# Optimization experiments

Hardware: AMD Instinct MI355X
Metric: run time of the kernel (lower is better)

The kernel has to match this reference:

```python
import jax, jax.numpy as jnp
import numpy as np

B, T, D, M, N = 32, 24, 32, 32, 32
H = 32           # hidden_dim (must equal D due to .view in the torch code)
C = M * N        # number of independent per-cell LSTMs
K = 3            # conv kernel size, padding = K // 2


def setup_inputs() -> dict:
    key = jax.random.key(0)
    ks = jax.random.split(key, 7)
    s = 1.0 / np.sqrt(H)  # torch nn.LSTM default init scale
    return {
        "x": jax.random.normal(ks[0], (B, T, D, M, N), jnp.float32),
        "W_ih": jax.random.uniform(ks[1], (C, 4 * H, D), jnp.float32, -s, s),
        "W_hh": jax.random.uniform(ks[2], (C, 4 * H, H), jnp.float32, -s, s),
        "b_ih": jax.random.uniform(ks[3], (C, 4 * H), jnp.float32, -s, s),
        "b_hh": jax.random.uniform(ks[4], (C, 4 * H), jnp.float32, -s, s),
        "conv_w": jax.random.normal(ks[5], (1, H, K, K), jnp.float32) * 0.05,
        "conv_b": jax.random.normal(ks[6], (1,), jnp.float32) * 0.05,
    }


def _spatial_lstm(x, W_ih, W_hh, b_ih, b_hh):
    # x: (B,T,D,M,N) -> per-cell sequences (T,C,B,D)
    xf = x.reshape(B, T, D, C).transpose(1, 3, 0, 2)
    bias = (b_ih + b_hh)[:, None, :]  # (C,1,4H)

    def step(carry, xt):
        h, c = carry  # (C,B,H)
        g = (jnp.einsum('cbd,cgd->cbg', xt, W_ih)
             + jnp.einsum('cbh,cgh->cbg', h, W_hh) + bias)
        i, f, gg, o = jnp.split(g, 4, axis=-1)  # torch gate order i,f,g,o
        c = jax.nn.sigmoid(f) * c + jax.nn.sigmoid(i) * jnp.tanh(gg)
        h = jax.nn.sigmoid(o) * jnp.tanh(c)
        return (h, c), h

    h0 = jnp.zeros((C, B, H), x.dtype)
    _, hs = jax.lax.scan(step, (h0, h0), xf)  # hs: (T,C,B,H)
    # stack over cells, view back to grid: (B,T,H,M,N)
    return hs.transpose(2, 0, 3, 1).reshape(B, T, H, M, N)


def reference(x, W_ih, W_hh, b_ih, b_hh, conv_w, conv_b):
    spatial = _spatial_lstm(x, W_ih, W_hh, b_ih, b_hh)  # (B,T,H,M,N)
    y = jax.lax.conv_general_dilated(
        spatial.reshape(B * T, H, M, N), conv_w,
        window_strides=(1, 1), padding=[(K // 2, K // 2)] * 2,
        dimension_numbers=('NCHW', 'OIHW', 'NCHW'))
    y = y + conv_b[None, :, None, None]
    return jax.nn.sigmoid(y).reshape(B, T, -1, M, N)


if __name__ == "__main__":
    out = reference(**setup_inputs())
    print(out.shape)
```

## Files before the change

### kernel.cpp

```cpp
#include <hip/hip_runtime.h>

#define Bn 32
#define Tn 24
#define Dn 32
#define Hn 32
#define Cn 1024
#define DC (Dn*Cn)
#define TDC (Tn*Dn*Cn)
#define MP 34
#define PPXN (MP*MP)
#define IMGS (MP*MP*32)
#define SCALE 1.442695041f

typedef __attribute__((ext_vector_type(8))) short bf16x8;
typedef __attribute__((ext_vector_type(4))) float f32x4;

__device__ __forceinline__ unsigned cvt_pk(float lo, float hi) {
    unsigned r; asm("v_cvt_pk_bf16_f32 %0, %1, %2" : "=v"(r) : "v"(lo), "v"(hi)); return r;
}
__device__ __forceinline__ float lo16f(unsigned u) { return __builtin_bit_cast(float, u << 16); }
__device__ __forceinline__ float hi16f(unsigned u) { return __builtin_bit_cast(float, u & 0xffff0000u); }
__device__ __forceinline__ float rcp_(float x) { return __builtin_amdgcn_rcpf(x); }
__device__ __forceinline__ float exp2_(float x) { return __builtin_amdgcn_exp2f(x); }
__device__ __forceinline__ bf16x8 bc(int4 v) { return __builtin_bit_cast(bf16x8, v); }

struct __align__(16) LdsT {
    unsigned short Xh[2][2][32][48];
    unsigned short Xl[2][2][32][48];
    float Hf[2][2][32][36];
};

__global__ __launch_bounds__(512)
void zero_halo(unsigned short* __restrict__ sp) {
    int gid = blockIdx.x * 512 + threadIdx.x;
    if (gid >= 3072 * 132) return;
    int plane = gid / 132;
    int r = gid - plane * 132;
    int m, n;
    if (r < 34)       { m = 0;      n = r; }
    else if (r < 68)  { m = 33;     n = r - 34; }
    else if (r < 100) { m = r - 67; n = 0; }
    else              { m = r - 99; n = 33; }
    int4 z = {0, 0, 0, 0};
    *(int4*)(sp + ((size_t)plane * PPXN + m * MP + n) * 8) = z;
}

__global__ __launch_bounds__(256) __attribute__((amdgpu_waves_per_eu(3, 3)))
void lstm_k12(const float* __restrict__ x,
              const float* __restrict__ Wih,
              const float* __restrict__ Whh,
              const float* __restrict__ bih,
              const float* __restrict__ bhh,
              unsigned short* __restrict__ sp)
{
    __shared__ LdsT lds;
    const int tid  = threadIdx.x;
    const int lane = tid & 63;
    const int wave = tid >> 6;
    const int ci   = wave >> 1;
    const int half = wave & 1;
    const int l16  = lane & 15;
    const int kg   = lane >> 4;
    const int bid  = blockIdx.x;
    const int cellbase = (bid & 7) * 128 + (bid >> 3) * 2;
    const int cell = cellbase + ci;

    int4 wihh[4], wihl[4], whhh[4], whhl[4];
    float biasr[4];
#pragma unroll
    for (int q = 0; q < 4; ++q) {
        const int g = q * 32 + half * 16 + l16;
        const float* wp = Wih + (size_t)cell * 4096 + g * 32 + kg * 8;
        const float* hp = Whh + (size_t)cell * 4096 + g * 32 + kg * 8;
        float wv[8], hv[8];
#pragma unroll
        for (int j = 0; j < 8; ++j) { wv[j] = wp[j] * SCALE; hv[j] = hp[j] * SCALE; }
        unsigned a0 = cvt_pk(wv[0], wv[1]), a1 = cvt_pk(wv[2], wv[3]);
        unsigned a2 = cvt_pk(wv[4], wv[5]), a3 = cvt_pk(wv[6], wv[7]);
        wihh[q] = int4{(int)a0, (int)a1, (int)a2, (int)a3};
        wihl[q] = int4{(int)cvt_pk(wv[0] - lo16f(a0), wv[1] - hi16f(a0)),
                       (int)cvt_pk(wv[2] - lo16f(a1), wv[3] - hi16f(a1)),
                       (int)cvt_pk(wv[4] - lo16f(a2), wv[5] - hi16f(a2)),
                       (int)cvt_pk(wv[6] - lo16f(a3), wv[7] - hi16f(a3))};
        unsigned b0 = cvt_pk(hv[0], hv[1]), b1 = cvt_pk(hv[2], hv[3]);
        unsigned b2 = cvt_pk(hv[4], hv[5]), b3 = cvt_pk(hv[6], hv[7]);
        whhh[q] = int4{(int)b0, (int)b1, (int)b2, (int)b3};
        whhl[q] = int4{(int)cvt_pk(hv[0] - lo16f(b0), hv[1] - hi16f(b0)),
                       (int)cvt_pk(hv[2] - lo16f(b1), hv[3] - hi16f(b1)),
                       (int)cvt_pk(hv[4] - lo16f(b2), hv[5] - hi16f(b2)),
                       (int)cvt_pk(hv[6] - lo16f(b3), hv[7] - hi16f(b3))};
        biasr[q] = (bih[cell * 128 + g] + bhh[cell * 128 + g]) * SCALE;
    }

    const int sb = tid >> 3;
    const int d0 = (tid & 7) * 4;
    const float* xg0 = x + (size_t)sb * TDC + (size_t)d0 * Cn + cellbase;

    const int sm = cell >> 5, sn = cell & 31;
    const int ppx = (sm + 1) * MP + (sn + 1);
    unsigned short* spb = sp + ((size_t)(half * 16 + l16) * Tn * 4 + kg) * (PPXN * 8)
                             + (size_t)ppx * 8;

    float hD[8] = {};
    float cst[8] = {};
    float2 nx[4];
#pragma unroll
    for (int k = 0; k < 4; ++k) nx[k] = *(const float2*)(xg0 + k * Cn);

    for (int t = 0; t < Tn; ++t) {
        const int bufi = t & 1;
#pragma unroll
        for (int cc = 0; cc < 2; ++cc) {
            float f0 = cc ? nx[0].y : nx[0].x;
            float f1 = cc ? nx[1].y : nx[1].x;
            float f2 = cc ? nx[2].y : nx[2].x;
            float f3 = cc ? nx[3].y : nx[3].x;
            unsigned a0 = cvt_pk(f0, f1), a1 = cvt_pk(f2, f3);
            float r0 = f0 - lo16f(a0), r1 = f1 - hi16f(a0);
            float r2 = f2 - lo16f(a1), r3 = f3 - hi16f(a1);
            int2 hi2 = {(int)a0, (int)a1};
            int2 lo2 = {(int)cvt_pk(r0, r1), (int)cvt_pk(r2, r3)};
            *(int2*)&lds.Xh[bufi][cc][sb][d0] = hi2;
            *(int2*)&lds.Xl[bufi][cc][sb][d0] = lo2;
        }
#pragma unroll
        for (int i = 0; i < 8; ++i) {
            int mt = i >> 2, r = i & 3;
            lds.Hf[bufi][ci][mt * 16 + kg * 4 + r][half * 16 + l16] = hD[i];
        }
        __syncthreads();

        if (t < Tn - 1) {
#pragma unroll
            for (int k = 0; k < 4; ++k)
                nx[k] = *(const float2*)(xg0 + (size_t)(t + 1) * DC + k * Cn);
        }

        unsigned sphi0 = 0, sphi1 = 0, sphi2 = 0, sphi3 = 0;
#pragma unroll
        for (int mt = 0; mt < 2; ++mt) {
            int4 xfh = *(const int4*)&lds.Xh[bufi][ci][mt * 16 + l16][kg * 8];
            int4 xfl = *(const int4*)&lds.Xl[bufi][ci][mt * 16 + l16][kg * 8];
            const float* hp = &lds.Hf[bufi][ci][mt * 16 + l16][kg * 8];
            float4 ha = *(const float4*)hp;
            float4 hb = *(const float4*)(hp + 4);
            unsigned p0 = cvt_pk(ha.x, ha.y), p1 = cvt_pk(ha.z, ha.w);
            unsigned p2 = cvt_pk(hb.x, hb.y), p3 = cvt_pk(hb.z, hb.w);
            int4 hfh = int4{(int)p0, (int)p1, (int)p2, (int)p3};
            int4 hfl = int4{(int)cvt_pk(ha.x - lo16f(p0), ha.y - hi16f(p0)),
                            (int)cvt_pk(ha.z - lo16f(p1), ha.w - hi16f(p1)),
                            (int)cvt_pk(hb.x - lo16f(p2), hb.y - hi16f(p2)),
                            (int)cvt_pk(hb.z - lo16f(p3), hb.w - hi16f(p3))};
            if (mt == half) { sphi0 = p0; sphi1 = p1; sphi2 = p2; sphi3 = p3; }

            f32x4 acc[4];
#pragma unroll
            for (int q = 0; q < 4; ++q) {
                f32x4 a = {biasr[q], biasr[q], biasr[q], biasr[q]};
                a = __builtin_amdgcn_mfma_f32_16x16x32_bf16(bc(xfh), bc(wihh[q]), a, 0, 0, 0);
                a = __builtin_amdgcn_mfma_f32_16x16x32_bf16(bc(xfl), bc(wihh[q]), a, 0, 0, 0);
                a = __builtin_amdgcn_mfma_f32_16x16x32_bf16(bc(xfh), bc(wihl[q]), a, 0, 0, 0);
                a = __builtin_amdgcn_mfma_f32_16x16x32_bf16(bc(hfh), bc(whhh[q]), a, 0, 0, 0);
                a = __builtin_amdgcn_mfma_f32_16x16x32_bf16(bc(hfl), bc(whhh[q]), a, 0, 0, 0);
                a = __builtin_amdgcn_mfma_f32_16x16x32_bf16(bc(hfh), bc(whhl[q]), a, 0, 0, 0);
                acc[q] = a;
            }
#pragma unroll
            for (int r = 0; r < 4; ++r) {
                float gi = acc[0][r], gf = acc[1][r];
                float gg = acc[2][r], go = acc[3][r];
                float ig = rcp_(1.f + exp2_(-gi));
                float fg = rcp_(1.f + exp2_(-gf));
                float gt = 1.f - 2.f * rcp_(1.f + exp2_(gg + gg));
                float og = rcp_(1.f + exp2_(-go));
                float c  = fg * cst[mt * 4 + r] + ig * gt;
                cst[mt * 4 + r] = c;
                float tc = 1.f - 2.f * rcp_(1.f + exp2_((2.f * SCALE) * c));
                hD[mt * 4 + r] = og * tc;
            }
        }

        if (t > 0) {
            int4 sv = {(int)sphi0, (int)sphi1, (int)sphi2, (int)sphi3};
            *(int4*)(spb + (size_t)(t - 1) * IMGS) = sv;
        }
    }

#pragma unroll
    for (int i = 0; i < 8; ++i) {
        int mt = i >> 2, r = i & 3;
        lds.Hf[0][ci][mt * 16 + kg * 4 + r][half * 16 + l16] = hD[i];
    }
    __syncthreads();
    {
        const float* hp = &lds.Hf[0][ci][half * 16 + l16][kg * 8];
        float4 ha = *(const float4*)hp;
        float4 hb = *(const float4*)(hp + 4);
        int4 sv = {(int)cvt_pk(ha.x, ha.y), (int)cvt_pk(ha.z, ha.w),
                   (int)cvt_pk(hb.x, hb.y), (int)cvt_pk(hb.z, hb.w)};
        *(int4*)(spb + (size_t)(Tn - 1) * IMGS) = sv;
    }
}

__global__ __launch_bounds__(512, 4)
void conv_k4(const unsigned short* __restrict__ sp,
             const float* __restrict__ cw,
             const float* __restrict__ cb,
             float* __restrict__ out)
{
    __shared__ float wlds[9][32];
    const int tid = threadIdx.x;
    const int img = blockIdx.x;
    if (tid < 288) wlds[tid >> 5][tid & 31] = cw[(tid & 31) * 9 + (tid >> 5)];
    __syncthreads();
    const float bias = cb[0];
    float acc[2] = {bias, bias};
    int ppx[2];
#pragma unroll
    for (int pk = 0; pk < 2; ++pk) {
        int px = tid + pk * 512;
        ppx[pk] = ((px >> 5) + 1) * MP + (px & 31) + 1;
    }
#pragma unroll
    for (int hc = 0; hc < 4; ++hc) {
        float4 wa[9], wb[9];
#pragma unroll
        for (int tap = 0; tap < 9; ++tap) {
            wa[tap] = *(const float4*)&wlds[tap][hc * 8];
            wb[tap] = *(const float4*)&wlds[tap][hc * 8 + 4];
        }
        const unsigned short* plane = sp + (size_t)(img * 4 + hc) * (PPXN * 8);
#pragma unroll
        for (int pk = 0; pk < 2; ++pk) {
            const unsigned short* base = plane + (size_t)ppx[pk] * 8;
            float a = acc[pk];
#pragma unroll
            for (int dm = -1; dm <= 1; ++dm)
#pragma unroll
                for (int dn = -1; dn <= 1; ++dn) {
                    const int tap = (dm + 1) * 3 + (dn + 1);
                    int4 v = *(const int4*)(base + (dm * MP + dn) * 8);
                    float4 w0 = wa[tap], w1 = wb[tap];
                    a = fmaf(lo16f((unsigned)v.x), w0.x, a);
                    a = fmaf(hi16f((unsigned)v.x), w0.y, a);
                    a = fmaf(lo16f((unsigned)v.y), w0.z, a);
                    a = fmaf(hi16f((unsigned)v.y), w0.w, a);
                    a = fmaf(lo16f((unsigned)v.z), w1.x, a);
                    a = fmaf(hi16f((unsigned)v.z), w1.y, a);
                    a = fmaf(lo16f((unsigned)v.w), w1.z, a);
                    a = fmaf(hi16f((unsigned)v.w), w1.w, a);
                }
            acc[pk] = a;
        }
    }
#pragma unroll
    for (int pk = 0; pk < 2; ++pk)
        out[(size_t)img * 1024 + tid + pk * 512] = rcp_(1.f + exp2_(-SCALE * acc[pk]));
}

extern "C" void kernel_launch(void* const* d_in, const int* in_sizes, int n_in,
                              void* d_out, int out_size, void* d_ws, size_t ws_size,
                              hipStream_t stream) {
    const float* x   = (const float*)d_in[0];
    const float* Wih = (const float*)d_in[1];
    const float* Whh = (const float*)d_in[2];
    const float* bih = (const float*)d_in[3];
    const float* bhh = (const float*)d_in[4];
    const float* cw  = (const float*)d_in[5];
    const float* cb  = (const float*)d_in[6];
    float* out = (float*)d_out;
    unsigned short* sp = (unsigned short*)d_ws;

    zero_halo<<<792, 512, 0, stream>>>(sp);
    lstm_k12<<<512, 256, 0, stream>>>(x, Wih, Whh, bih, bhh, sp);
    conv_k4<<<Bn * Tn, 512, 0, stream>>>(sp, cw, cb, out);
}
```

Baseline: 103.9 us.

## Drop x low-part split, split MFMA chains, and use a lighter LDS barrier

Stops computing and storing the bf16 residual of x, which removes one MFMA per gate and the Xl LDS array. The input-projection and recurrent MFMA chains now go into separate accumulators that are added at the end, shortening the dependent chain. __syncthreads is replaced with a custom barrier that waits only on LDS counters, so the next-step global x prefetch is no longer waited on at the barrier. Pointer increments replace the per-step index math. The precision of x·W_ih drops to the bf16 hi part times the split weights.

```diff
diff --git a/kernel.cpp b/kernel.cpp
--- a/kernel.cpp
+++ b/kernel.cpp
@@ -24,9 +24,12 @@
 __device__ __forceinline__ float exp2_(float x) { return __builtin_amdgcn_exp2f(x); }
 __device__ __forceinline__ bf16x8 bc(int4 v) { return __builtin_bit_cast(bf16x8, v); }
 
+__device__ __forceinline__ void lds_barrier() {
+    asm volatile("s_waitcnt lgkmcnt(0)\n\ts_barrier" ::: "memory");
+}
+
 struct __align__(16) LdsT {
     unsigned short Xh[2][2][32][48];
-    unsigned short Xl[2][2][32][48];
     float Hf[2][2][32][36];
 };
 
@@ -46,7 +49,7 @@
 }
 
 __global__ __launch_bounds__(256) __attribute__((amdgpu_waves_per_eu(3, 3)))
-void lstm_k12(const float* __restrict__ x,
+void lstm_k15(const float* __restrict__ x,
               const float* __restrict__ Wih,
               const float* __restrict__ Whh,
               const float* __restrict__ bih,
@@ -95,11 +98,12 @@
     const int sb = tid >> 3;
     const int d0 = (tid & 7) * 4;
     const float* xg0 = x + (size_t)sb * TDC + (size_t)d0 * Cn + cellbase;
+    const float* xcur = xg0 + DC;
 
     const int sm = cell >> 5, sn = cell & 31;
     const int ppx = (sm + 1) * MP + (sn + 1);
-    unsigned short* spb = sp + ((size_t)(half * 16 + l16) * Tn * 4 + kg) * (PPXN * 8)
-                             + (size_t)ppx * 8;
+    unsigned short* spcur = sp + ((size_t)(half * 16 + l16) * Tn * 4 + kg) * (PPXN * 8)
+                               + (size_t)ppx * 8;
 
     float hD[8] = {};
     float cst[8] = {};
@@ -115,32 +119,26 @@
             float f1 = cc ? nx[1].y : nx[1].x;
             float f2 = cc ? nx[2].y : nx[2].x;
             float f3 = cc ? nx[3].y : nx[3].x;
-            unsigned a0 = cvt_pk(f0, f1), a1 = cvt_pk(f2, f3);
-            float r0 = f0 - lo16f(a0), r1 = f1 - hi16f(a0);
-            float r2 = f2 - lo16f(a1), r3 = f3 - hi16f(a1);
-            int2 hi2 = {(int)a0, (int)a1};
-            int2 lo2 = {(int)cvt_pk(r0, r1), (int)cvt_pk(r2, r3)};
+            int2 hi2 = {(int)cvt_pk(f0, f1), (int)cvt_pk(f2, f3)};
             *(int2*)&lds.Xh[bufi][cc][sb][d0] = hi2;
-            *(int2*)&lds.Xl[bufi][cc][sb][d0] = lo2;
         }
 #pragma unroll
         for (int i = 0; i < 8; ++i) {
             int mt = i >> 2, r = i & 3;
             lds.Hf[bufi][ci][mt * 16 + kg * 4 + r][half * 16 + l16] = hD[i];
         }
-        __syncthreads();
-
         if (t < Tn - 1) {
 #pragma unroll
             for (int k = 0; k < 4; ++k)
-                nx[k] = *(const float2*)(xg0 + (size_t)(t + 1) * DC + k * Cn);
-        }
+                nx[k] = *(const float2*)(xcur + k * Cn);
+            xcur += DC;
+        }
+        lds_barrier();
 
         unsigned sphi0 = 0, sphi1 = 0, sphi2 = 0, sphi3 = 0;
 #pragma unroll
         for (int mt = 0; mt < 2; ++mt) {
             int4 xfh = *(const int4*)&lds.Xh[bufi][ci][mt * 16 + l16][kg * 8];
-            int4 xfl = *(const int4*)&lds.Xl[bufi][ci][mt * 16 + l16][kg * 8];
             const float* hp = &lds.Hf[bufi][ci][mt * 16 + l16][kg * 8];
             float4 ha = *(const float4*)hp;
             float4 hb = *(const float4*)(hp + 4);
@@ -156,14 +154,14 @@
             f32x4 acc[4];
 #pragma unroll
             for (int q = 0; q < 4; ++q) {
-                f32x4 a = {biasr[q], biasr[q], biasr[q], biasr[q]};
-                a = __builtin_amdgcn_mfma_f32_16x16x32_bf16(bc(xfh), bc(wihh[q]), a, 0, 0, 0);
-                a = __builtin_amdgcn_mfma_f32_16x16x32_bf16(bc(xfl), bc(wihh[q]), a, 0, 0, 0);
-                a = __builtin_amdgcn_mfma_f32_16x16x32_bf16(bc(xfh), bc(wihl[q]), a, 0, 0, 0);
-                a = __builtin_amdgcn_mfma_f32_16x16x32_bf16(bc(hfh), bc(whhh[q]), a, 0, 0, 0);
-                a = __builtin_amdgcn_mfma_f32_16x16x32_bf16(bc(hfl), bc(whhh[q]), a, 0, 0, 0);
-                a = __builtin_amdgcn_mfma_f32_16x16x32_bf16(bc(hfh), bc(whhl[q]), a, 0, 0, 0);
-                acc[q] = a;
+                f32x4 ax = {biasr[q], biasr[q], biasr[q], biasr[q]};
+                ax = __builtin_amdgcn_mfma_f32_16x16x32_bf16(bc(xfh), bc(wihh[q]), ax, 0, 0, 0);
+                ax = __builtin_amdgcn_mfma_f32_16x16x32_bf16(bc(xfh), bc(wihl[q]), ax, 0, 0, 0);
+                f32x4 ah = {0.f, 0.f, 0.f, 0.f};
+                ah = __builtin_amdgcn_mfma_f32_16x16x32_bf16(bc(hfh), bc(whhh[q]), ah, 0, 0, 0);
+                ah = __builtin_amdgcn_mfma_f32_16x16x32_bf16(bc(hfl), bc(whhh[q]), ah, 0, 0, 0);
+                ah = __builtin_amdgcn_mfma_f32_16x16x32_bf16(bc(hfh), bc(whhl[q]), ah, 0, 0, 0);
+                acc[q] = ax + ah;
             }
 #pragma unroll
             for (int r = 0; r < 4; ++r) {
@@ -182,7 +180,8 @@
 
         if (t > 0) {
             int4 sv = {(int)sphi0, (int)sphi1, (int)sphi2, (int)sphi3};
-            *(int4*)(spb + (size_t)(t - 1) * IMGS) = sv;
+            *(int4*)spcur = sv;
+            spcur += IMGS;
         }
     }
 
@@ -191,14 +190,14 @@
         int mt = i >> 2, r = i & 3;
         lds.Hf[0][ci][mt * 16 + kg * 4 + r][half * 16 + l16] = hD[i];
     }
-    __syncthreads();
+    lds_barrier();
     {
         const float* hp = &lds.Hf[0][ci][half * 16 + l16][kg * 8];
         float4 ha = *(const float4*)hp;
         float4 hb = *(const float4*)(hp + 4);
         int4 sv = {(int)cvt_pk(ha.x, ha.y), (int)cvt_pk(ha.z, ha.w),
                    (int)cvt_pk(hb.x, hb.y), (int)cvt_pk(hb.z, hb.w)};
-        *(int4*)(spb + (size_t)(Tn - 1) * IMGS) = sv;
+        *(int4*)spcur = sv;
     }
 }
 
@@ -272,6 +271,6 @@
     unsigned short* sp = (unsigned short*)d_ws;
 
     zero_halo<<<792, 512, 0, stream>>>(sp);
-    lstm_k12<<<512, 256, 0, stream>>>(x, Wih, Whh, bih, bhh, sp);
+    lstm_k15<<<512, 256, 0, stream>>>(x, Wih, Whh, bih, bhh, sp);
     conv_k4<<<Bn * Tn, 512, 0, stream>>>(sp, cw, cb, out);
 }
```

Measured after the change: 102.4 us. No clear change (-1.5%).
